# Performance work log

Measured on AMD Instinct MI355X. Metric: run time of the kernel, lower is better.

## Reference

```python
import jax, jax.numpy as jnp
import numpy as np
from jax import lax

S, B, VIN, VOUT, U, E = 64, 256, 128, 128, 1024, 512
START_CODE = 0
T_DEC = 25  # MAX_DECODE_STEPS


def gru_step(x, h, Wih, Whh, bih, bhh):
    # PyTorch GRU cell, gate order r,z,n
    gi = x @ Wih.T + bih
    gh = h @ Whh.T + bhh
    ir, iz, inn = jnp.split(gi, 3, axis=-1)
    hr, hz, hn = jnp.split(gh, 3, axis=-1)
    r = jax.nn.sigmoid(ir + hr)
    z = jax.nn.sigmoid(iz + hz)
    n = jnp.tanh(inn + r * hn)
    return (1.0 - z) * n + z * h


def setup_inputs() -> dict:
    key = jax.random.key(0)
    ks = jax.random.split(key, 20)
    sc = 0.05
    inp = {
        'x': jax.random.normal(ks[0], (S, B, VIN), jnp.float32),
        'x_len': jnp.maximum(jnp.sort(jax.random.randint(ks[1], (B,), 0, S + 1)), 1),
        'enc_Wih': jax.random.normal(ks[2], (3 * U, VIN), jnp.float32) * sc,
        'enc_Whh': jax.random.normal(ks[3], (3 * U, U), jnp.float32) * sc,
        'enc_bih': jnp.zeros((3 * U,), jnp.float32),
        'enc_bhh': jnp.zeros((3 * U,), jnp.float32),
        'dec_Wih': jax.random.normal(ks[4], (3 * U, E + U), jnp.float32) * sc,
        'dec_Whh': jax.random.normal(ks[5], (3 * U, U), jnp.float32) * sc,
        'dec_bih': jnp.zeros((3 * U,), jnp.float32),
        'dec_bhh': jnp.zeros((3 * U,), jnp.float32),
        'o2h_W': jax.random.normal(ks[6], (E, VOUT), jnp.float32) * sc,
        'o2h_b': jnp.zeros((E,), jnp.float32),
        'fc_W': jax.random.normal(ks[7], (VOUT, U), jnp.float32) * sc,
        'fc_b': jnp.zeros((VOUT,), jnp.float32),
        'W1_W': jax.random.normal(ks[8], (U, U), jnp.float32) * sc,
        'W1_b': jnp.zeros((U,), jnp.float32),
        'W2_W': jax.random.normal(ks[9], (U, U), jnp.float32) * sc,
        'W2_b': jnp.zeros((U,), jnp.float32),
        'V_W': jax.random.normal(ks[10], (1, U), jnp.float32) * sc,
        'V_b': jnp.zeros((1,), jnp.float32),
    }
    return inp


def _forward(x, x_len, enc_Wih, enc_Whh, enc_bih, enc_bhh,
             dec_Wih, dec_Whh, dec_bih, dec_bhh,
             o2h_W, o2h_b, fc_W, fc_b, W1_W, W1_b, W2_W, W2_b, V_W, V_b):
    # ---- Encoder GRU with length masking (pack/pad semantics) ----
    h0 = jnp.zeros((B, U), jnp.float32)
    t_idx = jnp.arange(S)

    def enc_step(h, inp_t):
        xt, t = inp_t
        mask = (t < x_len)[:, None]  # [B,1]
        hn = gru_step(xt, h, enc_Wih, enc_Whh, enc_bih, enc_bhh)
        h = jnp.where(mask, hn, h)
        out = jnp.where(mask, hn, 0.0)
        return h, out

    enc_hidden, enc_out = lax.scan(enc_step, h0, (x, t_idx))  # enc_out [S,B,U]
    enc_out = jnp.transpose(enc_out, (1, 0, 2))  # [B,S,U]

    # ---- Greedy decode (teacher_force=False), 25 steps ----
    enc_proj = enc_out @ W1_W.T + W1_b  # precompute W1(enc_output), [B,S,U]
    start = jnp.zeros((B, VOUT), jnp.float32).at[:, START_CODE].set(1.0)

    def dec_step(carry, _):
        h, dec_in = carry
        score = jnp.tanh(enc_proj + (h @ W2_W.T + W2_b)[:, None, :])  # [B,S,U]
        logits = score @ V_W.T + V_b  # [B,S,1]
        attn = jax.nn.softmax(logits, axis=1)
        ctx = jnp.sum(attn * enc_out, axis=1)  # [B,U]
        emb = dec_in @ o2h_W.T + o2h_b  # [B,E]
        gx = jnp.concatenate([ctx, emb], axis=-1)
        hn = gru_step(gx, h, dec_Wih, dec_Whh, dec_bih, dec_bhh)
        pred = hn @ fc_W.T + fc_b  # [B,VOUT]
        onehot = jax.nn.one_hot(jnp.argmax(pred, axis=-1), VOUT, dtype=pred.dtype)
        return (hn, lax.stop_gradient(onehot)), pred

    _, preds = lax.scan(dec_step, (enc_hidden, start), None, length=T_DEC - 1)
    return jnp.concatenate([start[None], preds], axis=0)  # [25,B,VOUT]


def reference(x, x_len, enc_Wih, enc_Whh, enc_bih, enc_bhh,
              dec_Wih, dec_Whh, dec_bih, dec_bhh,
              o2h_W, o2h_b, fc_W, fc_b, W1_W, W1_b, W2_W, W2_b, V_W, V_b):
    return _forward(x, x_len, enc_Wih, enc_Whh, enc_bih, enc_bhh,
                    dec_Wih, dec_Whh, dec_bih, dec_bhh,
                    o2h_W, o2h_b, fc_W, fc_b, W1_W, W1_b, W2_W, W2_b, V_W, V_b)
```

## Files before the change

kernel.cpp:

```cpp
#include <hip/hip_runtime.h>
#include <math.h>

#define SLEN 64
#define BATCH 256
#define VIND 128
#define VOUTD 128
#define UDIM 1024
#define EDIM 512
#define TDEC 25
#define GXW 1536
#define U3 3072
#define NSEG 12

typedef __attribute__((ext_vector_type(8))) short short8;
typedef __attribute__((ext_vector_type(4))) float f32x4;

#define MFMA(acc, A, B) acc = __builtin_amdgcn_mfma_f32_16x16x32_bf16((A), (B), (acc), 0, 0, 0)

__device__ __forceinline__ float sigm(float x) { return 1.f / (1.f + expf(-x)); }

__device__ __forceinline__ float tanhf_fast(float x) {
    float ax = fabsf(x);
    float e = __expf(-2.f * ax);
    float t = (1.f - e) / (1.f + e);
    return copysignf(t, x);
}

__device__ __forceinline__ short f2bf(float f) {
    unsigned u = __float_as_uint(f);
    u += 0x7FFF + ((u >> 16) & 1);
    return (short)(u >> 16);
}
__device__ __forceinline__ float bf2f(short h) {
    return __uint_as_float(((unsigned)(unsigned short)h) << 16);
}

__device__ __forceinline__ size_t pkChunk(int r, int k, int K) {
    return ((size_t)(r >> 4) * (K >> 5) + (k >> 5)) * 64 + ((r & 15) + 16 * ((k >> 3) & 3));
}

union S8 { short s[8]; short8 v; };

__device__ __forceinline__ void writeSplit8(short* Hi, short* Lo, size_t chunk,
                                            const float* vals) {
    S8 h, l;
#pragma unroll
    for (int j = 0; j < 8; j++) {
        short hb = f2bf(vals[j]);
        h.s[j] = hb;
        l.s[j] = f2bf(vals[j] - bf2f(hb));
    }
    ((short8*)Hi)[chunk] = h.v;
    ((short8*)Lo)[chunk] = l.v;
}

__global__ void init_kernel(float* __restrict__ h0, short* __restrict__ hpHi,
                            short* __restrict__ hpLo, float* __restrict__ out0,
                            int* __restrict__ idx) {
    int i = blockIdx.x * 256 + threadIdx.x;
    if (i < BATCH * UDIM) { h0[i] = 0.f; hpHi[i] = 0; hpLo[i] = 0; }
    if (i < BATCH * VOUTD) out0[i] = ((i & (VOUTD - 1)) == 0) ? 1.f : 0.f;
    if (i < BATCH) idx[i] = 0;
}

struct PackSeg {
    const float* sA; const float* sB;
    short* Hi; short* Lo;
    int KA, KB, offA, offB, chunkStart;
};
struct PackArgs { PackSeg s[NSEG]; };

__global__ void pack_all(PackArgs pa, int total) {
    int gid = blockIdx.x * 256 + threadIdx.x;
    if (gid >= total) return;
    int si = 0;
#pragma unroll
    for (int i = 1; i < NSEG; i++) si = (gid >= pa.s[i].chunkStart) ? i : si;
    PackSeg sg = pa.s[si];
    int local = gid - sg.chunkStart;
    int K = sg.KA + sg.KB;
    int cpr = K >> 3;
    int r = local / cpr, k0 = (local - r * cpr) * 8;
    const float* src = (k0 < sg.KA)
        ? sg.sA + (size_t)(sg.offA + r) * sg.KA + k0
        : sg.sB + (size_t)(sg.offB + r) * sg.KB + (k0 - sg.KA);
    float v[8];
#pragma unroll
    for (int j = 0; j < 8; j++) v[j] = src[j];
    writeSplit8(sg.Hi, sg.Lo, pkChunk(r, k0, K), v);
}

__global__ __launch_bounds__(256) void gemm_w(
    const short8* __restrict__ Ahi, const short8* __restrict__ Alo,
    const short8* __restrict__ Whi, const short8* __restrict__ Wlo,
    const float* __restrict__ bias, float* __restrict__ C,
    int KT, int N) {
    int tid = threadIdx.x, lane = tid & 63, wave = tid >> 6;
    int m16 = blockIdx.x * 4 + (wave & 1) * 2;
    int nb = blockIdx.y * 8 + (wave >> 1) * 4;
    const short8* a0h = Ahi + (size_t)m16 * KT * 64 + lane;
    const short8* a1h = a0h + (size_t)KT * 64;
    const short8* a0l = Alo + (size_t)m16 * KT * 64 + lane;
    const short8* a1l = a0l + (size_t)KT * 64;
    const short8* w0h = Whi + (size_t)(nb + 0) * KT * 64 + lane;
    const short8* w1h = Whi + (size_t)(nb + 1) * KT * 64 + lane;
    const short8* w2h = Whi + (size_t)(nb + 2) * KT * 64 + lane;
    const short8* w3h = Whi + (size_t)(nb + 3) * KT * 64 + lane;
    const short8* w0l = Wlo + (size_t)(nb + 0) * KT * 64 + lane;
    const short8* w1l = Wlo + (size_t)(nb + 1) * KT * 64 + lane;
    const short8* w2l = Wlo + (size_t)(nb + 2) * KT * 64 + lane;
    const short8* w3l = Wlo + (size_t)(nb + 3) * KT * 64 + lane;
    f32x4 acc0[4] = {}, acc1[4] = {};

    for (int kt = 0; kt < KT; kt++) {
        size_t o = (size_t)kt * 64;
        short8 A0H = a0h[o], A1H = a1h[o], A0L = a0l[o], A1L = a1l[o];
        short8 WH0 = w0h[o], WL0 = w0l[o];
        MFMA(acc0[0], A0H, WH0); MFMA(acc1[0], A1H, WH0);
        MFMA(acc0[0], A0H, WL0); MFMA(acc1[0], A1H, WL0);
        MFMA(acc0[0], A0L, WH0); MFMA(acc1[0], A1L, WH0);
        short8 WH1 = w1h[o], WL1 = w1l[o];
        MFMA(acc0[1], A0H, WH1); MFMA(acc1[1], A1H, WH1);
        MFMA(acc0[1], A0H, WL1); MFMA(acc1[1], A1H, WL1);
        MFMA(acc0[1], A0L, WH1); MFMA(acc1[1], A1L, WH1);
        short8 WH2 = w2h[o], WL2 = w2l[o];
        MFMA(acc0[2], A0H, WH2); MFMA(acc1[2], A1H, WH2);
        MFMA(acc0[2], A0H, WL2); MFMA(acc1[2], A1H, WL2);
        MFMA(acc0[2], A0L, WH2); MFMA(acc1[2], A1L, WH2);
        short8 WH3 = w3h[o], WL3 = w3l[o];
        MFMA(acc0[3], A0H, WH3); MFMA(acc1[3], A1H, WH3);
        MFMA(acc0[3], A0H, WL3); MFMA(acc1[3], A1H, WL3);
        MFMA(acc0[3], A0L, WH3); MFMA(acc1[3], A1L, WH3);
    }
    int rsub = (lane >> 4) * 4, cn = lane & 15;
    int row0 = (m16 + 0) * 16 + rsub;
    int row1 = (m16 + 1) * 16 + rsub;
#pragma unroll
    for (int j = 0; j < 4; j++) {
        int col = (nb + j) * 16 + cn;
        float bb = bias ? bias[col] : 0.f;
#pragma unroll
        for (int r = 0; r < 4; r++) {
            C[(size_t)(row0 + r) * N + col] = acc0[j][r] + bb;
            C[(size_t)(row1 + r) * N + col] = acc1[j][r] + bb;
        }
    }
}

__global__ __launch_bounds__(256) void gemm_bm32(
    const short8* __restrict__ Ahi, const short8* __restrict__ Alo,
    const short8* __restrict__ Whi, const short8* __restrict__ Wlo,
    const float* __restrict__ bias, float* __restrict__ C,
    int KT, int N) {
    int tid = threadIdx.x, lane = tid & 63, wave = tid >> 6;
    int m16 = blockIdx.x * 2 + (wave & 1);
    int n16 = blockIdx.y * 4 + (wave >> 1) * 2;
    const short8* ah = Ahi + (size_t)m16 * KT * 64 + lane;
    const short8* al = Alo + (size_t)m16 * KT * 64 + lane;
    const short8* w0h = Whi + (size_t)n16 * KT * 64 + lane;
    const short8* w1h = w0h + (size_t)KT * 64;
    const short8* w0l = Wlo + (size_t)n16 * KT * 64 + lane;
    const short8* w1l = w0l + (size_t)KT * 64;
    f32x4 a0 = {0,0,0,0}, a1 = {0,0,0,0};
    for (int kt = 0; kt < KT; kt++) {
        size_t o = (size_t)kt * 64;
        short8 AH = ah[o], AL = al[o];
        short8 W0H = w0h[o], W0L = w0l[o], W1H = w1h[o], W1L = w1l[o];
        MFMA(a0, AH, W0H); MFMA(a1, AH, W1H);
        MFMA(a0, AH, W0L); MFMA(a1, AH, W1L);
        MFMA(a0, AL, W0H); MFMA(a1, AL, W1H);
    }
    int rsub = (lane >> 4) * 4, cn = lane & 15;
    float b0 = bias ? bias[(n16 + 0) * 16 + cn] : 0.f;
    float b1 = bias ? bias[(n16 + 1) * 16 + cn] : 0.f;
#pragma unroll
    for (int r = 0; r < 4; r++) {
        int row = m16 * 16 + rsub + r;
        C[(size_t)row * N + (n16 + 0) * 16 + cn] = a0[r] + b0;
        C[(size_t)row * N + (n16 + 1) * 16 + cn] = a1[r] + b1;
    }
}

__global__ __launch_bounds__(192) void enc_gru3(
    const short8* __restrict__ hinH8, const short8* __restrict__ hinL8,
    const short8* __restrict__ WrH, const short8* __restrict__ WrL,
    const short8* __restrict__ WzH, const short8* __restrict__ WzL,
    const short8* __restrict__ WnH, const short8* __restrict__ WnL,
    const float* __restrict__ gi,
    const float* __restrict__ bih, const float* __restrict__ bhh,
    const float* __restrict__ hinF, float* __restrict__ houtF,
    short* __restrict__ hoH, short* __restrict__ hoL,
    short* __restrict__ eaHi, short* __restrict__ eaLo,
    const int* __restrict__ x_len, int t) {
    __shared__ float sC[3][16][16];
    __shared__ float sHo[16][16];
    __shared__ float sEo[16][16];
    int tid = threadIdx.x, lane = tid & 63, wave = tid >> 6;
    int g = blockIdx.x;
    int m16 = blockIdx.y;
    const short8* ah = hinH8 + (size_t)m16 * 32 * 64 + lane;
    const short8* al = hinL8 + (size_t)m16 * 32 * 64 + lane;
    const short8* wh;
    const short8* wl;
    if (wave == 0) { wh = WrH + (size_t)g * 32 * 64 + lane; wl = WrL + (size_t)g * 32 * 64 + lane; }
    else if (wave == 1) { wh = WzH + (size_t)g * 32 * 64 + lane; wl = WzL + (size_t)g * 32 * 64 + lane; }
    else { wh = WnH + (size_t)g * 32 * 64 + lane; wl = WnL + (size_t)g * 32 * 64 + lane; }
    f32x4 acc = {0, 0, 0, 0};
    for (int kt = 0; kt < 32; kt++) {
        size_t o = (size_t)kt * 64;
        short8 AH = ah[o], AL = al[o];
        short8 WH = wh[o], WL = wl[o];
        MFMA(acc, AH, WH);
        MFMA(acc, AH, WL);
        MFMA(acc, AL, WH);
    }
    {
        int rsub = (lane >> 4) << 2, cn = lane & 15;
#pragma unroll
        for (int j = 0; j < 4; j++) sC[wave][rsub + j][cn] = acc[j];
    }
    __syncthreads();
    if (wave == 0) {
        int cu = g * 16 + (lane & 15);
        int rsub = (lane >> 4) << 2;
        float b_r = bih[cu] + bhh[cu];
        float b_z = bih[UDIM + cu] + bhh[UDIM + cu];
        float b_nh = bhh[2 * UDIM + cu];
        float b_ni = bih[2 * UDIM + cu];
        int growLocal = (t & 7) * 256;
#pragma unroll
        for (int j = 0; j < 4; j++) {
            int b = m16 * 16 + rsub + j;
            const float* gr = gi + (size_t)(growLocal + b) * U3;
            float rg = sigm(sC[0][rsub + j][lane & 15] + gr[cu] + b_r);
            float zg = sigm(sC[1][rsub + j][lane & 15] + gr[UDIM + cu] + b_z);
            float nn = tanhf(gr[2 * UDIM + cu] + b_ni +
                             rg * (sC[2][rsub + j][lane & 15] + b_nh));
            float hp = hinF[(size_t)b * UDIM + cu];
            float hv = (1.f - zg) * nn + zg * hp;
            bool msk = t < x_len[b];
            float ho = msk ? hv : hp;
            houtF[(size_t)b * UDIM + cu] = ho;
            sHo[rsub + j][lane & 15] = ho;
            sEo[rsub + j][lane & 15] = msk ? hv : 0.f;
        }
    }
    __syncthreads();
    if (wave == 1 && lane < 32) {
        int rr = lane >> 1, oct = lane & 1;
        int brow = m16 * 16 + rr;
        int u0 = g * 16 + oct * 8;
        float v[8];
#pragma unroll
        for (int j = 0; j < 8; j++) v[j] = sHo[rr][oct * 8 + j];
        writeSplit8(hoH, hoL, pkChunk(brow, u0, UDIM), v);
#pragma unroll
        for (int j = 0; j < 8; j++) v[j] = sEo[rr][oct * 8 + j];
        writeSplit8(eaHi, eaLo, pkChunk(brow * SLEN + t, u0, UDIM), v);
    }
}

__global__ __launch_bounds__(192) void dec_gru3(
    const short8* __restrict__ hinH8, const short8* __restrict__ hinL8,
    const short8* __restrict__ gxH8, const short8* __restrict__ gxL8,
    const short8* __restrict__ WrH, const short8* __restrict__ WrL,
    const short8* __restrict__ WzH, const short8* __restrict__ WzL,
    const short8* __restrict__ WnhH, const short8* __restrict__ WnhL,
    const short8* __restrict__ WniH, const short8* __restrict__ WniL,
    const float* __restrict__ bih, const float* __restrict__ bhh,
    const float* __restrict__ hinF, float* __restrict__ houtF,
    short* __restrict__ hoH, short* __restrict__ hoL) {
    __shared__ float sC[4][16][16];
    __shared__ float sHo[16][16];
    int tid = threadIdx.x, lane = tid & 63, wave = tid >> 6;
    int g = blockIdx.x;
    int m16 = blockIdx.y;
    const short8* ah = hinH8 + (size_t)m16 * 32 * 64 + lane;
    const short8* al = hinL8 + (size_t)m16 * 32 * 64 + lane;
    const short8* gxh = gxH8 + (size_t)m16 * 48 * 64 + lane;
    const short8* gxl = gxL8 + (size_t)m16 * 48 * 64 + lane;
    const short8 *whA, *wlA, *whB, *wlB;
    if (wave == 0) {
        whA = WrH + (size_t)g * 80 * 64 + lane; wlA = WrL + (size_t)g * 80 * 64 + lane;
        whB = whA + 32 * 64; wlB = wlA + 32 * 64;
    } else if (wave == 1) {
        whA = WzH + (size_t)g * 80 * 64 + lane; wlA = WzL + (size_t)g * 80 * 64 + lane;
        whB = whA + 32 * 64; wlB = wlA + 32 * 64;
    } else {
        whA = WnhH + (size_t)g * 32 * 64 + lane; wlA = WnhL + (size_t)g * 32 * 64 + lane;
        whB = WniH + (size_t)g * 48 * 64 + lane; wlB = WniL + (size_t)g * 48 * 64 + lane;
    }
    f32x4 accA = {0,0,0,0}, accB = {0,0,0,0};
    for (int kt = 0; kt < 32; kt++) {
        size_t o = (size_t)kt * 64;
        short8 AH = ah[o], AL = al[o];
        short8 WH = whA[o], WL = wlA[o];
        MFMA(accA, AH, WH);
        MFMA(accA, AH, WL);
        MFMA(accA, AL, WH);
    }
    for (int kt = 0; kt < 48; kt++) {
        size_t o = (size_t)kt * 64;
        short8 AH = gxh[o], AL = gxl[o];
        short8 WH = whB[o], WL = wlB[o];
        MFMA(accB, AH, WH);
        MFMA(accB, AH, WL);
        MFMA(accB, AL, WH);
    }
    {
        int rsub = (lane >> 4) << 2, cn = lane & 15;
        if (wave < 2) {
#pragma unroll
            for (int j = 0; j < 4; j++) sC[wave][rsub + j][cn] = accA[j] + accB[j];
        } else {
#pragma unroll
            for (int j = 0; j < 4; j++) {
                sC[2][rsub + j][cn] = accA[j];
                sC[3][rsub + j][cn] = accB[j];
            }
        }
    }
    __syncthreads();
    if (wave == 0) {
        int cu = g * 16 + (lane & 15);
        int rsub = (lane >> 4) << 2;
        float b_r = bih[cu] + bhh[cu];
        float b_z = bih[UDIM + cu] + bhh[UDIM + cu];
        float b_nh = bhh[2 * UDIM + cu];
        float b_ni = bih[2 * UDIM + cu];
#pragma unroll
        for (int j = 0; j < 4; j++) {
            int b = m16 * 16 + rsub + j;
            float rg = sigm(sC[0][rsub + j][lane & 15] + b_r);
            float zg = sigm(sC[1][rsub + j][lane & 15] + b_z);
            float nn = tanhf(sC[3][rsub + j][lane & 15] + b_ni +
                             rg * (sC[2][rsub + j][lane & 15] + b_nh));
            float hp = hinF[(size_t)b * UDIM + cu];
            float hv = (1.f - zg) * nn + zg * hp;
            houtF[(size_t)b * UDIM + cu] = hv;
            sHo[rsub + j][lane & 15] = hv;
        }
    }
    __syncthreads();
    if (wave == 1 && lane < 32) {
        int rr = lane >> 1, oct = lane & 1;
        int brow = m16 * 16 + rr;
        int u0 = g * 16 + oct * 8;
        float v[8];
#pragma unroll
        for (int j = 0; j < 8; j++) v[j] = sHo[rr][oct * 8 + j];
        writeSplit8(hoH, hoL, pkChunk(brow, u0, UDIM), v);
    }
}

__global__ __launch_bounds__(256) void attn_ctx(
    const float* __restrict__ encProj,
    const short* __restrict__ eaHi, const short* __restrict__ eaLo,
    const float* __restrict__ tmp2, const float* __restrict__ V_W,
    const float* __restrict__ V_b,
    const float* __restrict__ o2h_W, const float* __restrict__ o2h_b,
    const int* __restrict__ idx, short* __restrict__ gxHi, short* __restrict__ gxLo) {
    int b = blockIdx.x;
    int tid = threadIdx.x, lane = tid & 63, wave = tid >> 6;
    __shared__ float s_t2[UDIM];
    __shared__ float s_v[UDIM];
    __shared__ float s_attn[SLEN];
    for (int u = tid; u < UDIM; u += 256) {
        s_t2[u] = tmp2[(size_t)b * UDIM + u];
        s_v[u] = V_W[u];
    }
    __syncthreads();
    for (int s = wave; s < SLEN; s += 4) {
        const float4* ep4 = (const float4*)(encProj + ((size_t)b * SLEN + s) * UDIM);
        float p = 0.f;
        for (int u4 = lane; u4 < UDIM / 4; u4 += 64) {
            float4 e = ep4[u4];
            int u = 4 * u4;
            p += tanhf_fast(e.x + s_t2[u]) * s_v[u] +
                 tanhf_fast(e.y + s_t2[u + 1]) * s_v[u + 1] +
                 tanhf_fast(e.z + s_t2[u + 2]) * s_v[u + 2] +
                 tanhf_fast(e.w + s_t2[u + 3]) * s_v[u + 3];
        }
#pragma unroll
        for (int off = 32; off > 0; off >>= 1) p += __shfl_xor(p, off);
        if (lane == 0) s_attn[s] = p + V_b[0];
    }
    __syncthreads();
    if (tid < 64) {
        float v = s_attn[tid];
        float mx = v;
#pragma unroll
        for (int off = 32; off > 0; off >>= 1) mx = fmaxf(mx, __shfl_xor(mx, off));
        float e = expf(v - mx);
        float sum = e;
#pragma unroll
        for (int off = 32; off > 0; off >>= 1) sum += __shfl_xor(sum, off);
        s_attn[tid] = e / sum;
    }
    __syncthreads();
    if (tid < 128) {
        int u0 = tid * 8;
        float a[8] = {0, 0, 0, 0, 0, 0, 0, 0};
        const short8* hi8 = (const short8*)eaHi;
        const short8* lo8 = (const short8*)eaLo;
        int lanePart = 16 * ((u0 >> 3) & 3);
        int colPart = u0 >> 5;
        for (int s = 0; s < SLEN; s++) {
            int r = b * SLEN + s;
            size_t ch = ((size_t)(r >> 4) * (UDIM >> 5) + colPart) * 64 + (r & 15) + lanePart;
            S8 h, l;
            h.v = hi8[ch];
            l.v = lo8[ch];
            float w = s_attn[s];
#pragma unroll
            for (int j = 0; j < 8; j++) a[j] += w * (bf2f(h.s[j]) + bf2f(l.s[j]));
        }
        writeSplit8(gxHi, gxLo, pkChunk(b, u0, GXW), a);
    } else if (tid < 192) {
        int e0 = (tid - 128) * 8;
        int ib = idx[b];
        float a[8];
#pragma unroll
        for (int j = 0; j < 8; j++)
            a[j] = o2h_W[(size_t)(e0 + j) * VOUTD + ib] + o2h_b[e0 + j];
        writeSplit8(gxHi, gxLo, pkChunk(b, UDIM + e0, GXW), a);
    }
}

__global__ __launch_bounds__(256) void fcw2(
    const short8* __restrict__ hHi, const short8* __restrict__ hLo,
    const short8* __restrict__ fcH, const short8* __restrict__ fcL,
    const float* __restrict__ fc_b, float* __restrict__ pred,
    int* __restrict__ idx,
    const short8* __restrict__ w2H, const short8* __restrict__ w2L,
    const float* __restrict__ W2_b, float* __restrict__ tmp2) {
    __shared__ float sP[16][129];
    int tid = threadIdx.x, lane = tid & 63, wave = tid >> 6;
    if (blockIdx.x < 16) {
        int fm = blockIdx.x;
        const short8* ah = hHi + (size_t)fm * 32 * 64 + lane;
        const short8* al = hLo + (size_t)fm * 32 * 64 + lane;
        int n0 = 2 * wave, n1 = 2 * wave + 1;
        const short8* w0h = fcH + (size_t)n0 * 32 * 64 + lane;
        const short8* w0l = fcL + (size_t)n0 * 32 * 64 + lane;
        const short8* w1h = fcH + (size_t)n1 * 32 * 64 + lane;
        const short8* w1l = fcL + (size_t)n1 * 32 * 64 + lane;
        f32x4 a0 = {0,0,0,0}, a1 = {0,0,0,0};
        for (int kt = 0; kt < 32; kt++) {
            size_t o = (size_t)kt * 64;
            short8 AH = ah[o], AL = al[o];
            short8 W0H = w0h[o], W0L = w0l[o], W1H = w1h[o], W1L = w1l[o];
            MFMA(a0, AH, W0H); MFMA(a1, AH, W1H);
            MFMA(a0, AH, W0L); MFMA(a1, AH, W1L);
            MFMA(a0, AL, W0H); MFMA(a1, AL, W1H);
        }
        int cn = lane & 15, rsub = (lane >> 4) << 2;
#pragma unroll
        for (int j = 0; j < 4; j++) {
            sP[rsub + j][n0 * 16 + cn] = a0[j] + fc_b[n0 * 16 + cn];
            sP[rsub + j][n1 * 16 + cn] = a1[j] + fc_b[n1 * 16 + cn];
        }
        __syncthreads();
        {
            int row = tid >> 4, c0 = (tid & 15) * 8;
            float* pr = pred + (size_t)(fm * 16 + row) * VOUTD;
#pragma unroll
            for (int j = 0; j < 8; j++) pr[c0 + j] = sP[row][c0 + j];
        }
        if (tid < 16) {
            float v = sP[tid][0];
            int bi = 0;
            for (int j = 1; j < VOUTD; j++) {
                float w = sP[tid][j];
                if (w > v) { v = w; bi = j; }
            }
            idx[fm * 16 + tid] = bi;
        }
    } else {
        int lin = blockIdx.x - 16;
        int bx = lin & 7, by = lin >> 3;
        int m16 = bx * 2 + (wave & 1);
        int n16 = by * 4 + (wave >> 1) * 2;
        const short8* ah = hHi + (size_t)m16 * 32 * 64 + lane;
        const short8* al = hLo + (size_t)m16 * 32 * 64 + lane;
        const short8* w0h = w2H + (size_t)n16 * 32 * 64 + lane;
        const short8* w1h = w0h + (size_t)32 * 64;
        const short8* w0l = w2L + (size_t)n16 * 32 * 64 + lane;
        const short8* w1l = w0l + (size_t)32 * 64;
        f32x4 a0 = {0,0,0,0}, a1 = {0,0,0,0};
        for (int kt = 0; kt < 32; kt++) {
            size_t o = (size_t)kt * 64;
            short8 AH = ah[o], AL = al[o];
            short8 W0H = w0h[o], W0L = w0l[o], W1H = w1h[o], W1L = w1l[o];
            MFMA(a0, AH, W0H); MFMA(a1, AH, W1H);
            MFMA(a0, AH, W0L); MFMA(a1, AH, W1L);
            MFMA(a0, AL, W0H); MFMA(a1, AL, W1H);
        }
        int rsub = (lane >> 4) * 4, cn = lane & 15;
        float b0 = W2_b[(n16 + 0) * 16 + cn];
        float b1 = W2_b[(n16 + 1) * 16 + cn];
#pragma unroll
        for (int r = 0; r < 4; r++) {
            int row = m16 * 16 + rsub + r;
            tmp2[(size_t)row * UDIM + (n16 + 0) * 16 + cn] = a0[r] + b0;
            tmp2[(size_t)row * UDIM + (n16 + 1) * 16 + cn] = a1[r] + b1;
        }
    }
}

extern "C" void kernel_launch(void* const* d_in, const int* in_sizes, int n_in,
                              void* d_out, int out_size, void* d_ws, size_t ws_size,
                              hipStream_t stream) {
    const float* x       = (const float*)d_in[0];
    const int*   x_len   = (const int*)d_in[1];
    const float* enc_Wih = (const float*)d_in[2];
    const float* enc_Whh = (const float*)d_in[3];
    const float* enc_bih = (const float*)d_in[4];
    const float* enc_bhh = (const float*)d_in[5];
    const float* dec_Wih = (const float*)d_in[6];
    const float* dec_Whh = (const float*)d_in[7];
    const float* dec_bih = (const float*)d_in[8];
    const float* dec_bhh = (const float*)d_in[9];
    const float* o2h_W   = (const float*)d_in[10];
    const float* o2h_b   = (const float*)d_in[11];
    const float* fc_W    = (const float*)d_in[12];
    const float* fc_b    = (const float*)d_in[13];
    const float* W1_W    = (const float*)d_in[14];
    const float* W1_b    = (const float*)d_in[15];
    const float* W2_W    = (const float*)d_in[16];
    const float* W2_b    = (const float*)d_in[17];
    const float* V_W     = (const float*)d_in[18];
    const float* V_b     = (const float*)d_in[19];
    float* out = (float*)d_out;

    char* p = (char*)d_ws;
    auto alloc = [&](size_t bytes) -> char* {
        char* q = p;
        p += (bytes + 255) & ~(size_t)255;
        return q;
    };
    float* hAF  = (float*)alloc((size_t)BATCH * UDIM * 4);
    float* hBF  = (float*)alloc((size_t)BATCH * UDIM * 4);
    short* hAH  = (short*)alloc((size_t)BATCH * UDIM * 2);
    short* hAL  = (short*)alloc((size_t)BATCH * UDIM * 2);
    short* hBH  = (short*)alloc((size_t)BATCH * UDIM * 2);
    short* hBL  = (short*)alloc((size_t)BATCH * UDIM * 2);
    float* tmp2 = (float*)alloc((size_t)BATCH * UDIM * 4);
    short* gxHi = (short*)alloc((size_t)BATCH * GXW * 2);
    short* gxLo = (short*)alloc((size_t)BATCH * GXW * 2);
    short* encAHi = (short*)alloc((size_t)BATCH * SLEN * UDIM * 2);
    short* encALo = (short*)alloc((size_t)BATCH * SLEN * UDIM * 2);
    float* encProjF = (float*)alloc((size_t)BATCH * SLEN * UDIM * 4);
    float* gihBuf = (float*)alloc((size_t)8 * BATCH * U3 * 4);
    short* eWihH = (short*)alloc((size_t)U3 * VIND * 2);
    short* eWihL = (short*)alloc((size_t)U3 * VIND * 2);
    short* eWrH = (short*)alloc((size_t)UDIM * UDIM * 2);
    short* eWrL = (short*)alloc((size_t)UDIM * UDIM * 2);
    short* eWzH = (short*)alloc((size_t)UDIM * UDIM * 2);
    short* eWzL = (short*)alloc((size_t)UDIM * UDIM * 2);
    short* eWnH = (short*)alloc((size_t)UDIM * UDIM * 2);
    short* eWnL = (short*)alloc((size_t)UDIM * UDIM * 2);
    short* dWrH = (short*)alloc((size_t)UDIM * 2560 * 2);
    short* dWrL = (short*)alloc((size_t)UDIM * 2560 * 2);
    short* dWzH = (short*)alloc((size_t)UDIM * 2560 * 2);
    short* dWzL = (short*)alloc((size_t)UDIM * 2560 * 2);
    short* dWnhH = (short*)alloc((size_t)UDIM * UDIM * 2);
    short* dWnhL = (short*)alloc((size_t)UDIM * UDIM * 2);
    short* dWniH = (short*)alloc((size_t)UDIM * GXW * 2);
    short* dWniL = (short*)alloc((size_t)UDIM * GXW * 2);
    short* w1Hi = (short*)alloc((size_t)UDIM * UDIM * 2);
    short* w1Lo = (short*)alloc((size_t)UDIM * UDIM * 2);
    short* w2Hi = (short*)alloc((size_t)UDIM * UDIM * 2);
    short* w2Lo = (short*)alloc((size_t)UDIM * UDIM * 2);
    short* fcHi = (short*)alloc((size_t)VOUTD * UDIM * 2);
    short* fcLo = (short*)alloc((size_t)VOUTD * UDIM * 2);
    short* xHi  = (short*)alloc((size_t)SLEN * BATCH * VIND * 2);
    short* xLo  = (short*)alloc((size_t)SLEN * BATCH * VIND * 2);
    int*   idx  = (int*)alloc(BATCH * 4);

    init_kernel<<<(BATCH * UDIM + 255) / 256, 256, 0, stream>>>(hAF, hAH, hAL, out, idx);

    {
        PackArgs pa;
        int cs = 0, n = 0;
        auto seg = [&](const float* sA, int KA, int offA, const float* sB, int KB,
                       int offB, short* Hi, short* Lo, int R) {
            pa.s[n] = {sA, sB, Hi, Lo, KA, KB, offA, offB, cs};
            cs += R * (KA + KB) / 8;
            n++;
        };
        seg(enc_Wih, VIND, 0, nullptr, 0, 0, eWihH, eWihL, U3);
        seg(enc_Whh, UDIM, 0, nullptr, 0, 0, eWrH, eWrL, UDIM);
        seg(enc_Whh, UDIM, UDIM, nullptr, 0, 0, eWzH, eWzL, UDIM);
        seg(enc_Whh, UDIM, 2 * UDIM, nullptr, 0, 0, eWnH, eWnL, UDIM);
        seg(dec_Whh, UDIM, 0, dec_Wih, GXW, 0, dWrH, dWrL, UDIM);
        seg(dec_Whh, UDIM, UDIM, dec_Wih, GXW, UDIM, dWzH, dWzL, UDIM);
        seg(dec_Whh, UDIM, 2 * UDIM, nullptr, 0, 0, dWnhH, dWnhL, UDIM);
        seg(dec_Wih, GXW, 2 * UDIM, nullptr, 0, 0, dWniH, dWniL, UDIM);
        seg(W1_W, UDIM, 0, nullptr, 0, 0, w1Hi, w1Lo, UDIM);
        seg(W2_W, UDIM, 0, nullptr, 0, 0, w2Hi, w2Lo, UDIM);
        seg(fc_W, UDIM, 0, nullptr, 0, 0, fcHi, fcLo, VOUTD);
        seg(x, VIND, 0, nullptr, 0, 0, xHi, xLo, SLEN * BATCH);
        pack_all<<<(cs + 255) / 256, 256, 0, stream>>>(pa, cs);
    }

    float* hcF = hAF; float* hnF = hBF;
    short *hcH = hAH, *hcL = hAL, *hnH = hBH, *hnL = hBL;
    for (int c = 0; c < 8; c++) {
        gemm_w<<<dim3(32, 24), 256, 0, stream>>>(
            (const short8*)xHi + (size_t)c * 128 * 4 * 64,
            (const short8*)xLo + (size_t)c * 128 * 4 * 64,
            (const short8*)eWihH, (const short8*)eWihL,
            nullptr, gihBuf, VIND / 32, U3);
        for (int tt = 0; tt < 8; tt++) {
            int t = c * 8 + tt;
            enc_gru3<<<dim3(64, 16), 192, 0, stream>>>(
                (const short8*)hcH, (const short8*)hcL,
                (const short8*)eWrH, (const short8*)eWrL,
                (const short8*)eWzH, (const short8*)eWzL,
                (const short8*)eWnH, (const short8*)eWnL,
                gihBuf, enc_bih, enc_bhh, hcF, hnF, hnH, hnL,
                encAHi, encALo, x_len, t);
            { float* tf = hcF; hcF = hnF; hnF = tf; }
            { short* th = hcH; hcH = hnH; hnH = th; th = hcL; hcL = hnL; hnL = th; }
        }
    }

    gemm_w<<<dim3(SLEN * BATCH / 64, UDIM / 128), 256, 0, stream>>>(
        (const short8*)encAHi, (const short8*)encALo,
        (const short8*)w1Hi, (const short8*)w1Lo,
        W1_b, encProjF, UDIM / 32, UDIM);

    gemm_bm32<<<dim3(BATCH / 32, UDIM / 64), 256, 0, stream>>>(
        (const short8*)hcH, (const short8*)hcL,
        (const short8*)w2Hi, (const short8*)w2Lo,
        W2_b, tmp2, UDIM / 32, UDIM);

    for (int st = 0; st < TDEC - 1; st++) {
        attn_ctx<<<BATCH, 256, 0, stream>>>(
            encProjF, encAHi, encALo, tmp2, V_W, V_b, o2h_W, o2h_b, idx, gxHi, gxLo);
        dec_gru3<<<dim3(64, 16), 192, 0, stream>>>(
            (const short8*)hcH, (const short8*)hcL,
            (const short8*)gxHi, (const short8*)gxLo,
            (const short8*)dWrH, (const short8*)dWrL,
            (const short8*)dWzH, (const short8*)dWzL,
            (const short8*)dWnhH, (const short8*)dWnhL,
            (const short8*)dWniH, (const short8*)dWniL,
            dec_bih, dec_bhh, hcF, hnF, hnH, hnL);
        float* pred = out + (size_t)(1 + st) * BATCH * VOUTD;
        fcw2<<<144, 256, 0, stream>>>(
            (const short8*)hnH, (const short8*)hnL,
            (const short8*)fcHi, (const short8*)fcLo,
            fc_b, pred, idx,
            (const short8*)w2Hi, (const short8*)w2Lo, W2_b, tmp2);
        { float* tf = hcF; hcF = hnF; hnF = tf; }
        { short* th = hcH; hcH = hnH; hnH = th; th = hcL; hcL = hnL; hnL = th; }
    }
}
```

Before: 4.165 ms.

## Split GRU K-reduction across wave pairs, widen attention block, parallelize argmax

The encoder and decoder GRU kernels now use 6 waves instead of 3, with each gate's K-loop split in half across two waves and the partial sums combined in shared memory. The attention kernel uses 1024 threads, so the context reduction over sequence positions is split into 8 groups and summed through shared memory. The o2h embedding is pre-transposed with its bias folded in during init, so rows can be read contiguously. The fc argmax is spread over 8 lanes per row with a shuffle reduction. The goal is to shorten the serial latency of these latency-bound per-step kernels, at the cost of extra shared-memory traffic and higher per-block thread counts.

```diff
diff --git a/kernel.cpp b/kernel.cpp
--- a/kernel.cpp
+++ b/kernel.cpp
@@ -56,11 +56,18 @@
 
 __global__ void init_kernel(float* __restrict__ h0, short* __restrict__ hpHi,
                             short* __restrict__ hpLo, float* __restrict__ out0,
-                            int* __restrict__ idx) {
+                            int* __restrict__ idx,
+                            const float* __restrict__ o2h_W,
+                            const float* __restrict__ o2h_b,
+                            float* __restrict__ o2hT) {
     int i = blockIdx.x * 256 + threadIdx.x;
     if (i < BATCH * UDIM) { h0[i] = 0.f; hpHi[i] = 0; hpLo[i] = 0; }
     if (i < BATCH * VOUTD) out0[i] = ((i & (VOUTD - 1)) == 0) ? 1.f : 0.f;
     if (i < BATCH) idx[i] = 0;
+    if (i < VOUTD * EDIM) {
+        int v = i >> 9, e = i & (EDIM - 1);
+        o2hT[i] = o2h_W[(size_t)e * VOUTD + v] + o2h_b[e];
+    }
 }
 
 struct PackSeg {
@@ -181,7 +188,7 @@
     }
 }
 
-__global__ __launch_bounds__(192) void enc_gru3(
+__global__ __launch_bounds__(384) void enc_gru3(
     const short8* __restrict__ hinH8, const short8* __restrict__ hinL8,
     const short8* __restrict__ WrH, const short8* __restrict__ WrL,
     const short8* __restrict__ WzH, const short8* __restrict__ WzL,
@@ -192,21 +199,21 @@
     short* __restrict__ hoH, short* __restrict__ hoL,
     short* __restrict__ eaHi, short* __restrict__ eaLo,
     const int* __restrict__ x_len, int t) {
-    __shared__ float sC[3][16][16];
+    __shared__ float sC[6][16][16];
     __shared__ float sHo[16][16];
     __shared__ float sEo[16][16];
     int tid = threadIdx.x, lane = tid & 63, wave = tid >> 6;
     int g = blockIdx.x;
     int m16 = blockIdx.y;
-    const short8* ah = hinH8 + (size_t)m16 * 32 * 64 + lane;
-    const short8* al = hinL8 + (size_t)m16 * 32 * 64 + lane;
-    const short8* wh;
-    const short8* wl;
-    if (wave == 0) { wh = WrH + (size_t)g * 32 * 64 + lane; wl = WrL + (size_t)g * 32 * 64 + lane; }
-    else if (wave == 1) { wh = WzH + (size_t)g * 32 * 64 + lane; wl = WzL + (size_t)g * 32 * 64 + lane; }
-    else { wh = WnH + (size_t)g * 32 * 64 + lane; wl = WnL + (size_t)g * 32 * 64 + lane; }
+    int gate = wave >> 1, half = wave & 1;
+    const short8* ah = hinH8 + (size_t)m16 * 32 * 64 + (size_t)half * 16 * 64 + lane;
+    const short8* al = hinL8 + (size_t)m16 * 32 * 64 + (size_t)half * 16 * 64 + lane;
+    const short8* WH0 = (gate == 0) ? WrH : (gate == 1) ? WzH : WnH;
+    const short8* WL0 = (gate == 0) ? WrL : (gate == 1) ? WzL : WnL;
+    const short8* wh = WH0 + (size_t)g * 32 * 64 + (size_t)half * 16 * 64 + lane;
+    const short8* wl = WL0 + (size_t)g * 32 * 64 + (size_t)half * 16 * 64 + lane;
     f32x4 acc = {0, 0, 0, 0};
-    for (int kt = 0; kt < 32; kt++) {
+    for (int kt = 0; kt < 16; kt++) {
         size_t o = (size_t)kt * 64;
         short8 AH = ah[o], AL = al[o];
         short8 WH = wh[o], WL = wl[o];
@@ -230,19 +237,20 @@
         int growLocal = (t & 7) * 256;
 #pragma unroll
         for (int j = 0; j < 4; j++) {
-            int b = m16 * 16 + rsub + j;
+            int rr = rsub + j, cc = lane & 15;
+            int b = m16 * 16 + rr;
             const float* gr = gi + (size_t)(growLocal + b) * U3;
-            float rg = sigm(sC[0][rsub + j][lane & 15] + gr[cu] + b_r);
-            float zg = sigm(sC[1][rsub + j][lane & 15] + gr[UDIM + cu] + b_z);
+            float rg = sigm(sC[0][rr][cc] + sC[1][rr][cc] + gr[cu] + b_r);
+            float zg = sigm(sC[2][rr][cc] + sC[3][rr][cc] + gr[UDIM + cu] + b_z);
             float nn = tanhf(gr[2 * UDIM + cu] + b_ni +
-                             rg * (sC[2][rsub + j][lane & 15] + b_nh));
+                             rg * (sC[4][rr][cc] + sC[5][rr][cc] + b_nh));
             float hp = hinF[(size_t)b * UDIM + cu];
             float hv = (1.f - zg) * nn + zg * hp;
             bool msk = t < x_len[b];
             float ho = msk ? hv : hp;
             houtF[(size_t)b * UDIM + cu] = ho;
-            sHo[rsub + j][lane & 15] = ho;
-            sEo[rsub + j][lane & 15] = msk ? hv : 0.f;
+            sHo[rr][cc] = ho;
+            sEo[rr][cc] = msk ? hv : 0.f;
         }
     }
     __syncthreads();
@@ -260,7 +268,7 @@
     }
 }
 
-__global__ __launch_bounds__(192) void dec_gru3(
+__global__ __launch_bounds__(384) void dec_gru3(
     const short8* __restrict__ hinH8, const short8* __restrict__ hinL8,
     const short8* __restrict__ gxH8, const short8* __restrict__ gxL8,
     const short8* __restrict__ WrH, const short8* __restrict__ WrL,
@@ -270,28 +278,35 @@
     const float* __restrict__ bih, const float* __restrict__ bhh,
     const float* __restrict__ hinF, float* __restrict__ houtF,
     short* __restrict__ hoH, short* __restrict__ hoL) {
-    __shared__ float sC[4][16][16];
+    __shared__ float sC[8][16][16];
     __shared__ float sHo[16][16];
     int tid = threadIdx.x, lane = tid & 63, wave = tid >> 6;
     int g = blockIdx.x;
     int m16 = blockIdx.y;
-    const short8* ah = hinH8 + (size_t)m16 * 32 * 64 + lane;
-    const short8* al = hinL8 + (size_t)m16 * 32 * 64 + lane;
-    const short8* gxh = gxH8 + (size_t)m16 * 48 * 64 + lane;
-    const short8* gxl = gxL8 + (size_t)m16 * 48 * 64 + lane;
+    int gate = wave >> 1, half = wave & 1;
+    const short8* ah = hinH8 + (size_t)m16 * 32 * 64 + (size_t)half * 16 * 64 + lane;
+    const short8* al = hinL8 + (size_t)m16 * 32 * 64 + (size_t)half * 16 * 64 + lane;
+    const short8* gxh = gxH8 + (size_t)m16 * 48 * 64 + (size_t)half * 24 * 64 + lane;
+    const short8* gxl = gxL8 + (size_t)m16 * 48 * 64 + (size_t)half * 24 * 64 + lane;
     const short8 *whA, *wlA, *whB, *wlB;
-    if (wave == 0) {
-        whA = WrH + (size_t)g * 80 * 64 + lane; wlA = WrL + (size_t)g * 80 * 64 + lane;
-        whB = whA + 32 * 64; wlB = wlA + 32 * 64;
-    } else if (wave == 1) {
-        whA = WzH + (size_t)g * 80 * 64 + lane; wlA = WzL + (size_t)g * 80 * 64 + lane;
-        whB = whA + 32 * 64; wlB = wlA + 32 * 64;
+    if (gate == 0) {
+        whA = WrH + (size_t)g * 80 * 64 + (size_t)half * 16 * 64 + lane;
+        wlA = WrL + (size_t)g * 80 * 64 + (size_t)half * 16 * 64 + lane;
+        whB = WrH + (size_t)g * 80 * 64 + (size_t)(32 + half * 24) * 64 + lane;
+        wlB = WrL + (size_t)g * 80 * 64 + (size_t)(32 + half * 24) * 64 + lane;
+    } else if (gate == 1) {
+        whA = WzH + (size_t)g * 80 * 64 + (size_t)half * 16 * 64 + lane;
+        wlA = WzL + (size_t)g * 80 * 64 + (size_t)half * 16 * 64 + lane;
+        whB = WzH + (size_t)g * 80 * 64 + (size_t)(32 + half * 24) * 64 + lane;
+        wlB = WzL + (size_t)g * 80 * 64 + (size_t)(32 + half * 24) * 64 + lane;
     } else {
-        whA = WnhH + (size_t)g * 32 * 64 + lane; wlA = WnhL + (size_t)g * 32 * 64 + lane;
-        whB = WniH + (size_t)g * 48 * 64 + lane; wlB = WniL + (size_t)g * 48 * 64 + lane;
+        whA = WnhH + (size_t)g * 32 * 64 + (size_t)half * 16 * 64 + lane;
+        wlA = WnhL + (size_t)g * 32 * 64 + (size_t)half * 16 * 64 + lane;
+        whB = WniH + (size_t)g * 48 * 64 + (size_t)half * 24 * 64 + lane;
+        wlB = WniL + (size_t)g * 48 * 64 + (size_t)half * 24 * 64 + lane;
     }
     f32x4 accA = {0,0,0,0}, accB = {0,0,0,0};
-    for (int kt = 0; kt < 32; kt++) {
+    for (int kt = 0; kt < 16; kt++) {
         size_t o = (size_t)kt * 64;
         short8 AH = ah[o], AL = al[o];
         short8 WH = whA[o], WL = wlA[o];
@@ -299,7 +314,7 @@
         MFMA(accA, AH, WL);
         MFMA(accA, AL, WH);
     }
-    for (int kt = 0; kt < 48; kt++) {
+    for (int kt = 0; kt < 24; kt++) {
         size_t o = (size_t)kt * 64;
         short8 AH = gxh[o], AL = gxl[o];
         short8 WH = whB[o], WL = wlB[o];
@@ -309,14 +324,14 @@
     }
     {
         int rsub = (lane >> 4) << 2, cn = lane & 15;
-        if (wave < 2) {
+        if (wave < 4) {
 #pragma unroll
             for (int j = 0; j < 4; j++) sC[wave][rsub + j][cn] = accA[j] + accB[j];
         } else {
 #pragma unroll
             for (int j = 0; j < 4; j++) {
-                sC[2][rsub + j][cn] = accA[j];
-                sC[3][rsub + j][cn] = accB[j];
+                sC[wave][rsub + j][cn] = accA[j];
+                sC[wave + 2][rsub + j][cn] = accB[j];
             }
         }
     }
@@ -330,15 +345,16 @@
         float b_ni = bih[2 * UDIM + cu];
 #pragma unroll
         for (int j = 0; j < 4; j++) {
-            int b = m16 * 16 + rsub + j;
-            float rg = sigm(sC[0][rsub + j][lane & 15] + b_r);
-            float zg = sigm(sC[1][rsub + j][lane & 15] + b_z);
-            float nn = tanhf(sC[3][rsub + j][lane & 15] + b_ni +
-                             rg * (sC[2][rsub + j][lane & 15] + b_nh));
+            int rr = rsub + j, cc = lane & 15;
+            int b = m16 * 16 + rr;
+            float rg = sigm(sC[0][rr][cc] + sC[1][rr][cc] + b_r);
+            float zg = sigm(sC[2][rr][cc] + sC[3][rr][cc] + b_z);
+            float nn = tanhf(sC[6][rr][cc] + sC[7][rr][cc] + b_ni +
+                             rg * (sC[4][rr][cc] + sC[5][rr][cc] + b_nh));
             float hp = hinF[(size_t)b * UDIM + cu];
             float hv = (1.f - zg) * nn + zg * hp;
             houtF[(size_t)b * UDIM + cu] = hv;
-            sHo[rsub + j][lane & 15] = hv;
+            sHo[rr][cc] = hv;
         }
     }
     __syncthreads();
@@ -353,24 +369,25 @@
     }
 }
 
-__global__ __launch_bounds__(256) void attn_ctx(
+__global__ __launch_bounds__(1024) void attn_ctx(
     const float* __restrict__ encProj,
     const short* __restrict__ eaHi, const short* __restrict__ eaLo,
     const float* __restrict__ tmp2, const float* __restrict__ V_W,
     const float* __restrict__ V_b,
-    const float* __restrict__ o2h_W, const float* __restrict__ o2h_b,
+    const float* __restrict__ o2hT,
     const int* __restrict__ idx, short* __restrict__ gxHi, short* __restrict__ gxLo) {
     int b = blockIdx.x;
     int tid = threadIdx.x, lane = tid & 63, wave = tid >> 6;
     __shared__ float s_t2[UDIM];
     __shared__ float s_v[UDIM];
     __shared__ float s_attn[SLEN];
-    for (int u = tid; u < UDIM; u += 256) {
+    __shared__ float s_part[7][128][9];
+    for (int u = tid; u < UDIM; u += 1024) {
         s_t2[u] = tmp2[(size_t)b * UDIM + u];
         s_v[u] = V_W[u];
     }
     __syncthreads();
-    for (int s = wave; s < SLEN; s += 4) {
+    for (int s = wave; s < SLEN; s += 16) {
         const float4* ep4 = (const float4*)(encProj + ((size_t)b * SLEN + s) * UDIM);
         float p = 0.f;
         for (int u4 = lane; u4 < UDIM / 4; u4 += 64) {
@@ -398,14 +415,15 @@
         s_attn[tid] = e / sum;
     }
     __syncthreads();
-    if (tid < 128) {
-        int u0 = tid * 8;
+    {
+        int grp = tid >> 7, tu = tid & 127;
+        int u0 = tu * 8;
         float a[8] = {0, 0, 0, 0, 0, 0, 0, 0};
         const short8* hi8 = (const short8*)eaHi;
         const short8* lo8 = (const short8*)eaLo;
         int lanePart = 16 * ((u0 >> 3) & 3);
         int colPart = u0 >> 5;
-        for (int s = 0; s < SLEN; s++) {
+        for (int s = grp * 8; s < grp * 8 + 8; s++) {
             int r = b * SLEN + s;
             size_t ch = ((size_t)(r >> 4) * (UDIM >> 5) + colPart) * 64 + (r & 15) + lanePart;
             S8 h, l;
@@ -415,15 +433,26 @@
 #pragma unroll
             for (int j = 0; j < 8; j++) a[j] += w * (bf2f(h.s[j]) + bf2f(l.s[j]));
         }
-        writeSplit8(gxHi, gxLo, pkChunk(b, u0, GXW), a);
-    } else if (tid < 192) {
-        int e0 = (tid - 128) * 8;
-        int ib = idx[b];
-        float a[8];
-#pragma unroll
-        for (int j = 0; j < 8; j++)
-            a[j] = o2h_W[(size_t)(e0 + j) * VOUTD + ib] + o2h_b[e0 + j];
-        writeSplit8(gxHi, gxLo, pkChunk(b, UDIM + e0, GXW), a);
+        if (grp) {
+#pragma unroll
+            for (int j = 0; j < 8; j++) s_part[grp - 1][tu][j] = a[j];
+        }
+        __syncthreads();
+        if (tid < 128) {
+#pragma unroll
+            for (int gg = 0; gg < 7; gg++)
+#pragma unroll
+                for (int j = 0; j < 8; j++) a[j] += s_part[gg][tu][j];
+            writeSplit8(gxHi, gxLo, pkChunk(b, u0, GXW), a);
+        } else if (tid < 192) {
+            int e0 = (tid - 128) * 8;
+            int ib = idx[b];
+            const float* row = o2hT + (size_t)ib * EDIM + e0;
+            float v[8];
+#pragma unroll
+            for (int j = 0; j < 8; j++) v[j] = row[j];
+            writeSplit8(gxHi, gxLo, pkChunk(b, UDIM + e0, GXW), v);
+        }
     }
 }
 
@@ -467,14 +496,22 @@
 #pragma unroll
             for (int j = 0; j < 8; j++) pr[c0 + j] = sP[row][c0 + j];
         }
-        if (tid < 16) {
-            float v = sP[tid][0];
+        if (tid < 128) {
+            int row = tid >> 3, seg = tid & 7;
+            float v = -1e30f;
             int bi = 0;
-            for (int j = 1; j < VOUTD; j++) {
-                float w = sP[tid][j];
+            int c0 = seg * 16;
+            for (int j = c0; j < c0 + 16; j++) {
+                float w = sP[row][j];
                 if (w > v) { v = w; bi = j; }
             }
-            idx[fm * 16 + tid] = bi;
+#pragma unroll
+            for (int off = 1; off < 8; off <<= 1) {
+                float ov = __shfl_xor(v, off);
+                int obi = __shfl_xor(bi, off);
+                if (ov > v || (ov == v && obi < bi)) { v = ov; bi = obi; }
+            }
+            if (seg == 0) idx[fm * 16 + row] = bi;
         }
     } else {
         int lin = blockIdx.x - 16;
@@ -577,8 +614,10 @@
     short* xHi  = (short*)alloc((size_t)SLEN * BATCH * VIND * 2);
     short* xLo  = (short*)alloc((size_t)SLEN * BATCH * VIND * 2);
     int*   idx  = (int*)alloc(BATCH * 4);
-
-    init_kernel<<<(BATCH * UDIM + 255) / 256, 256, 0, stream>>>(hAF, hAH, hAL, out, idx);
+    float* o2hT = (float*)alloc((size_t)VOUTD * EDIM * 4);
+
+    init_kernel<<<(BATCH * UDIM + 255) / 256, 256, 0, stream>>>(
+        hAF, hAH, hAL, out, idx, o2h_W, o2h_b, o2hT);
 
     {
         PackArgs pa;
@@ -614,7 +653,7 @@
             nullptr, gihBuf, VIND / 32, U3);
         for (int tt = 0; tt < 8; tt++) {
             int t = c * 8 + tt;
-            enc_gru3<<<dim3(64, 16), 192, 0, stream>>>(
+            enc_gru3<<<dim3(64, 16), 384, 0, stream>>>(
                 (const short8*)hcH, (const short8*)hcL,
                 (const short8*)eWrH, (const short8*)eWrL,
                 (const short8*)eWzH, (const short8*)eWzL,
@@ -637,9 +676,9 @@
         W2_b, tmp2, UDIM / 32, UDIM);
 
     for (int st = 0; st < TDEC - 1; st++) {
-        attn_ctx<<<BATCH, 256, 0, stream>>>(
-            encProjF, encAHi, encALo, tmp2, V_W, V_b, o2h_W, o2h_b, idx, gxHi, gxLo);
-        dec_gru3<<<dim3(64, 16), 192, 0, stream>>>(
+        attn_ctx<<<BATCH, 1024, 0, stream>>>(
+            encProjF, encAHi, encALo, tmp2, V_W, V_b, o2hT, idx, gxHi, gxLo);
+        dec_gru3<<<dim3(64, 16), 384, 0, stream>>>(
             (const short8*)hcH, (const short8*)hcL,
             (const short8*)gxHi, (const short8*)gxLo,
             (const short8*)dWrH, (const short8*)dWrL,
```

Result: no change. 4.143 ms (-0.5%).
